# Kernel optimization log

Hardware: AMD Instinct MI355X
Metric: run time of the kernel (lower is better)

Reference implementation:

```python
import jax, jax.numpy as jnp
import numpy as np

N_NODES = 100000
N_EDGES = 1600000
IN_F = 128
OUT_F = 32
HEADS = 2
NEG_SLOPE = 0.2  # DGL GATConv default leaky_relu negative slope


def setup_inputs() -> dict:
    key = jax.random.key(0)
    ks = jax.random.split(key, 12)
    x = jax.random.normal(ks[0], (N_NODES, IN_F), dtype=jnp.float32)
    src = jax.random.randint(ks[1], (N_EDGES,), 0, N_NODES, dtype=jnp.int32)
    dst = jax.random.randint(ks[2], (N_EDGES,), 0, N_NODES, dtype=jnp.int32)
    # GATConv params: fc weight [IN_F, HEADS*OUT_F], attn_l/attn_r [HEADS, OUT_F], bias [HEADS*OUT_F]
    s = 1.0 / np.sqrt(IN_F)
    W = jax.random.normal(ks[3], (IN_F, HEADS * OUT_F), dtype=jnp.float32) * s
    attn_l = jax.random.normal(ks[4], (HEADS, OUT_F), dtype=jnp.float32) * s
    attn_r = jax.random.normal(ks[5], (HEADS, OUT_F), dtype=jnp.float32) * s
    bias_gat = jnp.zeros((HEADS * OUT_F,), dtype=jnp.float32)
    # MLPPredictor: lin1 (2*OUT_F -> OUT_F), lin2 (OUT_F -> 1)
    s1 = 1.0 / np.sqrt(2 * OUT_F)
    W1 = jax.random.normal(ks[6], (2 * OUT_F, OUT_F), dtype=jnp.float32) * s1
    b1 = jnp.zeros((OUT_F,), dtype=jnp.float32)
    s2 = 1.0 / np.sqrt(OUT_F)
    W2 = jax.random.normal(ks[7], (OUT_F, 1), dtype=jnp.float32) * s2
    b2 = jnp.zeros((1,), dtype=jnp.float32)
    return {"x": x, "W": W, "attn_l": attn_l, "attn_r": attn_r,
            "bias_gat": bias_gat, "W1": W1, "b1": b1, "W2": W2, "b2": b2,
            "src": src, "dst": dst}


def _forward(x, W, attn_l, attn_r, bias_gat, W1, b1, W2, b2, src, dst):
    # --- GATConv(in, out, 2 heads) ---
    feat = (x @ W).reshape(N_NODES, HEADS, OUT_F)           # [N,H,F]
    el = jnp.einsum('nhf,hf->nh', feat, attn_l)             # [N,H]
    er = jnp.einsum('nhf,hf->nh', feat, attn_r)             # [N,H]
    e = jax.nn.leaky_relu(el[src] + er[dst], NEG_SLOPE)     # [E,H]
    # edge softmax over incoming edges of each dst node (numerically stable)
    m = jax.ops.segment_max(e, dst, num_segments=N_NODES)   # [N,H]
    ex = jnp.exp(e - m[dst])                                # [E,H]
    denom = jax.ops.segment_sum(ex, dst, num_segments=N_NODES)  # [N,H]
    alpha = ex / denom[dst]                                 # [E,H]
    msg = feat[src] * alpha[:, :, None]                     # [E,H,F]
    rst = jax.ops.segment_sum(msg, dst, num_segments=N_NODES)   # [N,H,F]
    rst = rst + bias_gat.reshape(HEADS, OUT_F)
    h = jax.nn.relu(jnp.mean(rst, axis=1))                  # [N,F]
    # --- MLPPredictor: per-edge concat(src,dst) -> lin1 -> lin2 (no activation) ---
    hcat = jnp.concatenate([h[src], h[dst]], axis=1)        # [E,2F]
    score = (hcat @ W1 + b1) @ W2 + b2                      # [E,1]
    return score


def reference(x, W, attn_l, attn_r, bias_gat, W1, b1, W2, b2, src, dst):
    return _forward(x, W, attn_l, attn_r, bias_gat, W1, b1, W2, b2, src, dst)
```

## Files before the change

kernel.cpp:

```cpp
#include <hip/hip_runtime.h>
#include <hip/hip_fp16.h>

#define N_NODES 100000
#define N_EDGES 1600000
#define IN_F 128
#define OUT_F 32
#define HEADS 2
#define HO 64

#define NBUCK2 1563
#define BIN_BLOCKS 256
#define BIN_THREADS 1024
#define EPB (N_EDGES / BIN_BLOCKS)
#define NPT 7
#define LCAPH 1216

typedef __attribute__((ext_vector_type(8))) _Float16 half8;
typedef __attribute__((ext_vector_type(4))) _Float16 half4v;
typedef __attribute__((ext_vector_type(4))) float    f32x4;

#define XPAD 136

__global__ __launch_bounds__(256) void feat_k(
                       const float* __restrict__ x, const float* __restrict__ W,
                       const float* __restrict__ attn_l, const float* __restrict__ attn_r,
                       __half* __restrict__ feat16, float* __restrict__ el, float* __restrict__ er){
  __shared__ __align__(16) _Float16 Ws[64*XPAD];
  __shared__ __align__(16) _Float16 xs[64*XPAD];
  int tid = threadIdx.x;
  int node0 = blockIdx.x*64;

  for (int i = tid; i < 2048; i += 256){
    int k = i >> 4, c4 = (i & 15)*4;
    float4 v = ((const float4*)W)[i];
    Ws[(c4+0)*XPAD + k] = (_Float16)v.x;
    Ws[(c4+1)*XPAD + k] = (_Float16)v.y;
    Ws[(c4+2)*XPAD + k] = (_Float16)v.z;
    Ws[(c4+3)*XPAD + k] = (_Float16)v.w;
  }
  for (int i = tid; i < 2048; i += 256){
    int ln = i >> 5, kq = i & 31;
    int n = node0 + ln;
    float4 v = (n < N_NODES) ? ((const float4*)x)[(size_t)n*32 + kq]
                             : make_float4(0.f,0.f,0.f,0.f);
    half4v hv = { (_Float16)v.x, (_Float16)v.y, (_Float16)v.z, (_Float16)v.w };
    *(half4v*)&xs[ln*XPAD + kq*4] = hv;
  }
  __syncthreads();

  int w = tid >> 6, lane = tid & 63;
  int row_base = w*16;
  int lr = lane & 15, lg = lane >> 4;
  f32x4 acc0 = {0.f,0.f,0.f,0.f}, acc1 = {0.f,0.f,0.f,0.f};
  f32x4 acc2 = {0.f,0.f,0.f,0.f}, acc3 = {0.f,0.f,0.f,0.f};

  #pragma unroll
  for (int kk = 0; kk < 4; ++kk){
    int ko = kk*32 + lg*8;
    half8 a  = *(const half8*)&xs[(row_base + lr)*XPAD + ko];
    half8 b0 = *(const half8*)&Ws[( 0 + lr)*XPAD + ko];
    half8 b1 = *(const half8*)&Ws[(16 + lr)*XPAD + ko];
    half8 b2 = *(const half8*)&Ws[(32 + lr)*XPAD + ko];
    half8 b3 = *(const half8*)&Ws[(48 + lr)*XPAD + ko];
    acc0 = __builtin_amdgcn_mfma_f32_16x16x32_f16(a, b0, acc0, 0, 0, 0);
    acc1 = __builtin_amdgcn_mfma_f32_16x16x32_f16(a, b1, acc1, 0, 0, 0);
    acc2 = __builtin_amdgcn_mfma_f32_16x16x32_f16(a, b2, acc2, 0, 0, 0);
    acc3 = __builtin_amdgcn_mfma_f32_16x16x32_f16(a, b3, acc3, 0, 0, 0);
  }

  float al0 = attn_l[ 0 + lr], al1 = attn_l[16 + lr];
  float al2 = attn_l[32 + lr], al3 = attn_l[48 + lr];
  float ar0 = attn_r[ 0 + lr], ar1 = attn_r[16 + lr];
  float ar2 = attn_r[32 + lr], ar3 = attn_r[48 + lr];

  #pragma unroll
  for (int r = 0; r < 4; ++r){
    int n = node0 + row_base + lg*4 + r;
    float f0 = acc0[r], f1 = acc1[r], f2 = acc2[r], f3 = acc3[r];
    float p0 = f0*al0 + f1*al1, p1 = f2*al2 + f3*al3;
    float q0 = f0*ar0 + f1*ar1, q1 = f2*ar2 + f3*ar3;
    #pragma unroll
    for (int off = 1; off < 16; off <<= 1){
      p0 += __shfl_xor(p0, off); p1 += __shfl_xor(p1, off);
      q0 += __shfl_xor(q0, off); q1 += __shfl_xor(q1, off);
    }
    if (n < N_NODES){
      size_t base = (size_t)n*HO;
      feat16[base +  0 + lr] = __float2half_rn(f0);
      feat16[base + 16 + lr] = __float2half_rn(f1);
      feat16[base + 32 + lr] = __float2half_rn(f2);
      feat16[base + 48 + lr] = __float2half_rn(f3);
      if (lr == 0){
        *(float2*)&el[n*HEADS] = make_float2(p0, p1);
        *(float2*)&er[n*HEADS] = make_float2(q0, q1);
      }
    }
  }
}

__global__ __launch_bounds__(1024) void binB_k(const int* __restrict__ src,
                      const int* __restrict__ dst,
                      const float* __restrict__ el, const float* __restrict__ er,
                      const float* __restrict__ b1, const float* __restrict__ W2,
                      const float* __restrict__ b2,
                      int* __restrict__ bstart, float* __restrict__ ccomb,
                      uint2* __restrict__ stg){
  __shared__ int cnt[NBUCK2];
  int tid = threadIdx.x, blk = blockIdx.x;
  int lane = tid & 63, w = tid >> 6;
  if (blk == 0 && tid == 0){
    float a = 0.f;
    for (int k = 0; k < OUT_F; ++k) a = fmaf(b1[k], W2[k], a);
    *ccomb = a + b2[0];
  }
  for (int i = tid; i < NBUCK2; i += BIN_THREADS) cnt[i] = 0;
  __syncthreads();

  unsigned rx[NPT], rex[NPT];
  int rb[NPT];
  int ebase = blk*EPB;
  #pragma unroll
  for (int u = 0; u < NPT; ++u){
    int idx = tid + u*BIN_THREADS;
    rb[u] = -1;
    if (idx < EPB){
      int s = src[ebase + idx];
      int d = dst[ebase + idx];
      float2 elv = *(const float2*)&el[s*HEADS];
      float2 erv = *(const float2*)&er[d*HEADS];
      float t0 = elv.x + erv.x, t1 = elv.y + erv.y;
      t0 = t0 > 0.f ? t0 : 0.2f*t0;
      t1 = t1 > 0.f ? t1 : 0.2f*t1;
      __half2 ex2 = __float22half2_rn(make_float2(__expf(t0), __expf(t1)));
      int b = d >> 6;
      rb[u] = b;
      rx[u] = ((unsigned)s << 6) | (unsigned)(d & 63);
      rex[u] = *(const unsigned*)&ex2;
      atomicAdd(&cnt[b], 1);
    }
  }
  __syncthreads();

  if (w == 0){
    int run = 0;
    for (int c = 0; c < NBUCK2; c += 64){
      int i = c + lane;
      int v = (i < NBUCK2) ? cnt[i] : 0;
      int inc = v;
      #pragma unroll
      for (int off = 1; off < 64; off <<= 1){
        int t = __shfl_up(inc, off);
        if (lane >= off) inc += t;
      }
      if (i < NBUCK2) cnt[i] = run + inc - v;
      run += __shfl(inc, 63);
    }
  }
  __syncthreads();

  for (int i = tid; i < NBUCK2; i += BIN_THREADS)
    bstart[(size_t)blk*NBUCK2 + i] = cnt[i];
  __syncthreads();

  #pragma unroll
  for (int u = 0; u < NPT; ++u){
    if (rb[u] >= 0){
      int pos = atomicAdd(&cnt[rb[u]], 1);
      stg[(size_t)blk*EPB + pos] = make_uint2(rx[u], rex[u]);
    }
  }
}

__global__ void __launch_bounds__(512, 8) scatter_agg_k(
                              const int* __restrict__ bstart, const uint2* __restrict__ stg,
                              const __half* __restrict__ feat16, const float* __restrict__ bias,
                              const float* __restrict__ W1, const float* __restrict__ W2,
                              float* __restrict__ s1, float* __restrict__ s2){
  __shared__ uint2 lsev[LCAPH];
  __shared__ int soff[BIN_BLOCKS];
  __shared__ int send[BIN_BLOCKS];
  __shared__ float wc[64];
  __shared__ int hist[64];
  __shared__ int start_[64];
  __shared__ int cur[64];
  int b = blockIdx.x;
  int tid = threadIdx.x;
  int w = tid >> 6, lane = tid & 63;
  if (tid < 64){
    hist[tid] = 0;
    float a = 0.f;
    #pragma unroll
    for (int k = 0; k < OUT_F; ++k) a = fmaf(W1[tid*OUT_F + k], W2[k], a);
    wc[tid] = a;
  }
  for (int i = tid; i < BIN_BLOCKS; i += 512){
    int o = bstart[(size_t)i*NBUCK2 + b];
    int e = (b == NBUCK2-1) ? EPB : bstart[(size_t)i*NBUCK2 + b + 1];
    soff[i] = o; send[i] = e;
  }
  __syncthreads();

  int grp = tid >> 3, gl = tid & 7;

  for (int sg = grp; sg < BIN_BLOCKS; sg += 64){
    const uint2* seg = stg + (size_t)sg*EPB;
    int e = send[sg];
    for (int j = soff[sg] + gl; j < e; j += 8)
      atomicAdd(&hist[seg[j].x & 63], 1);
  }
  __syncthreads();

  if (tid < 64){
    int v = hist[tid];
    int inc = v;
    #pragma unroll
    for (int off = 1; off < 64; off <<= 1){
      int t = __shfl_up(inc, off);
      if (lane >= off) inc += t;
    }
    start_[tid] = inc - v;
    cur[tid] = inc - v;
  }
  __syncthreads();

  for (int sg = grp; sg < BIN_BLOCKS; sg += 64){
    const uint2* seg = stg + (size_t)sg*EPB;
    int e = send[sg];
    for (int j = soff[sg] + gl; j < e; j += 8){
      uint2 r = seg[j];
      int pos = atomicAdd(&cur[r.x & 63], 1);
      if (pos < LCAPH) lsev[pos] = make_uint2(r.x >> 6, r.y);
    }
  }
  __syncthreads();

  int g  = lane >> 4;
  int c4 = lane & 15;
  int h  = (c4 >= 8);
  float b0v = bias[c4*4 + 0], b1v = bias[c4*4 + 1], b2v = bias[c4*4 + 2], b3v = bias[c4*4 + 3];
  int f0 = (c4 & 7)*4;
  int wo = (h ? 32 : 0) + f0;
  float m0 = wc[wo], m1 = wc[wo+1], m2 = wc[wo+2], m3 = wc[wo+3];
  for (int i = 0; i < 8; ++i){
    int nl = w*8 + i;
    int node = b*64 + nl;
    if (node >= N_NODES) break;
    int s0 = start_[nl];
    int e0 = cur[nl]; if (e0 > LCAPH) e0 = LCAPH;
    int deg = e0 - s0; if (deg < 0) deg = 0;

    float a0=0.f, a1=0.f, a2=0.f, a3=0.f, dn=0.f;
    for (int j0 = 0; j0 < deg; j0 += 16){
      int jA = j0 + g, jB = j0 + 4 + g, jC = j0 + 8 + g, jD = j0 + 12 + g;
      float alA=0.f, alB=0.f, alC=0.f, alD=0.f;
      int snA=0, snB=0, snC=0, snD=0;
      if (jA < deg){ uint2 r = lsev[s0+jA]; snA = r.x;
        float2 e = __half22float2(*(const __half2*)&r.y); alA = (h?e.y:e.x); }
      if (jB < deg){ uint2 r = lsev[s0+jB]; snB = r.x;
        float2 e = __half22float2(*(const __half2*)&r.y); alB = (h?e.y:e.x); }
      if (jC < deg){ uint2 r = lsev[s0+jC]; snC = r.x;
        float2 e = __half22float2(*(const __half2*)&r.y); alC = (h?e.y:e.x); }
      if (jD < deg){ uint2 r = lsev[s0+jD]; snD = r.x;
        float2 e = __half22float2(*(const __half2*)&r.y); alD = (h?e.y:e.x); }
      dn += alA + alB + alC + alD;
      uint2 vA = *(const uint2*)(feat16 + (size_t)snA*HO + c4*4);
      uint2 vB = *(const uint2*)(feat16 + (size_t)snB*HO + c4*4);
      uint2 vC = *(const uint2*)(feat16 + (size_t)snC*HO + c4*4);
      uint2 vD = *(const uint2*)(feat16 + (size_t)snD*HO + c4*4);
      float2 fA01 = __half22float2(*(const __half2*)&vA.x);
      float2 fA23 = __half22float2(*(const __half2*)&vA.y);
      float2 fB01 = __half22float2(*(const __half2*)&vB.x);
      float2 fB23 = __half22float2(*(const __half2*)&vB.y);
      float2 fC01 = __half22float2(*(const __half2*)&vC.x);
      float2 fC23 = __half22float2(*(const __half2*)&vC.y);
      float2 fD01 = __half22float2(*(const __half2*)&vD.x);
      float2 fD23 = __half22float2(*(const __half2*)&vD.y);
      a0 = fmaf(alA, fA01.x, a0); a0 = fmaf(alB, fB01.x, a0);
      a0 = fmaf(alC, fC01.x, a0); a0 = fmaf(alD, fD01.x, a0);
      a1 = fmaf(alA, fA01.y, a1); a1 = fmaf(alB, fB01.y, a1);
      a1 = fmaf(alC, fC01.y, a1); a1 = fmaf(alD, fD01.y, a1);
      a2 = fmaf(alA, fA23.x, a2); a2 = fmaf(alB, fB23.x, a2);
      a2 = fmaf(alC, fC23.x, a2); a2 = fmaf(alD, fD23.x, a2);
      a3 = fmaf(alA, fA23.y, a3); a3 = fmaf(alB, fB23.y, a3);
      a3 = fmaf(alC, fC23.y, a3); a3 = fmaf(alD, fD23.y, a3);
    }
    a0 += __shfl_xor(a0, 16); a1 += __shfl_xor(a1, 16);
    a2 += __shfl_xor(a2, 16); a3 += __shfl_xor(a3, 16);
    dn += __shfl_xor(dn, 16);
    a0 += __shfl_xor(a0, 32); a1 += __shfl_xor(a1, 32);
    a2 += __shfl_xor(a2, 32); a3 += __shfl_xor(a3, 32);
    dn += __shfl_xor(dn, 32);
    float rh = dn > 0.f ? 1.f/dn : 0.f;
    a0 = fmaf(a0, rh, b0v); a1 = fmaf(a1, rh, b1v);
    a2 = fmaf(a2, rh, b2v); a3 = fmaf(a3, rh, b3v);
    float h0 = 0.5f*(a0 + __shfl_xor(a0, 8)); h0 = fmaxf(h0, 0.f);
    float h1 = 0.5f*(a1 + __shfl_xor(a1, 8)); h1 = fmaxf(h1, 0.f);
    float h2 = 0.5f*(a2 + __shfl_xor(a2, 8)); h2 = fmaxf(h2, 0.f);
    float h3 = 0.5f*(a3 + __shfl_xor(a3, 8)); h3 = fmaxf(h3, 0.f);
    float r = h0*m0 + h1*m1 + h2*m2 + h3*m3;
    r += __shfl_xor(r, 4); r += __shfl_xor(r, 2); r += __shfl_xor(r, 1);
    if (lane == 0)      s1[node] = r;
    else if (lane == 8) s2[node] = r;
  }
}

__global__ void edge_score_k(const int* __restrict__ src, const int* __restrict__ dst,
                             const float* __restrict__ s1, const float* __restrict__ s2,
                             const float* __restrict__ ccomb, float* __restrict__ out){
  int i = blockIdx.x*blockDim.x + threadIdx.x;
  if (i >= N_EDGES/4) return;
  int4 s4 = ((const int4*)src)[i];
  int4 d4 = ((const int4*)dst)[i];
  float c = ccomb[0];
  float4 o;
  o.x = s1[s4.x] + s2[d4.x] + c;
  o.y = s1[s4.y] + s2[d4.y] + c;
  o.z = s1[s4.z] + s2[d4.z] + c;
  o.w = s1[s4.w] + s2[d4.w] + c;
  ((float4*)out)[i] = o;
}

extern "C" void kernel_launch(void* const* d_in, const int* in_sizes, int n_in,
                              void* d_out, int out_size, void* d_ws, size_t ws_size,
                              hipStream_t stream){
  const float* x      = (const float*)d_in[0];
  const float* W      = (const float*)d_in[1];
  const float* attn_l = (const float*)d_in[2];
  const float* attn_r = (const float*)d_in[3];
  const float* bias   = (const float*)d_in[4];
  const float* W1     = (const float*)d_in[5];
  const float* b1     = (const float*)d_in[6];
  const float* W2     = (const float*)d_in[7];
  const float* b2     = (const float*)d_in[8];
  const int*   src    = (const int*)d_in[9];
  const int*   dst    = (const int*)d_in[10];
  float* out = (float*)d_out;

  float* ws = (float*)d_ws;
  size_t off = 0;
  __half* feat16 = (__half*)(ws + off); off += (size_t)N_NODES*HO/2;
  float*  el     = ws + off; off += (size_t)N_NODES*HEADS;
  float*  er     = ws + off; off += (size_t)N_NODES*HEADS;
  float*  s1     = ws + off; off += N_NODES;
  float*  s2     = ws + off; off += N_NODES;
  float*  ccomb  = ws + off; off += 64;
  int*    bstart = (int*)(ws + off); off += (size_t)BIN_BLOCKS*NBUCK2;
  off = (off + 1) & ~(size_t)1;
  uint2*  stg    = (uint2*)(ws + off); off += (size_t)2*N_EDGES;

  feat_k<<<(N_NODES + 63)/64, 256, 0, stream>>>(x, W, attn_l, attn_r, feat16, el, er);
  binB_k<<<BIN_BLOCKS, BIN_THREADS, 0, stream>>>(src, dst, el, er, b1, W2, b2,
                                                 bstart, ccomb, stg);
  scatter_agg_k<<<NBUCK2, 512, 0, stream>>>(bstart, stg, feat16, bias, W1, W2, s1, s2);
  edge_score_k<<<(N_EDGES/4 + 255)/256, 256, 0, stream>>>(src, dst, s1, s2, ccomb, out);
}
```

Before: 223.3 us.

## Vectorize binning loads, stage bucket edges once in LDS, widen edge-score kernel

The binning kernel now uses 250 blocks so each block's edge count splits evenly into int4 loads of src/dst, and it batches all gather loads before computing. The scatter-aggregate kernel computes per-segment offsets with a prefix scan and copies staged edges into LDS once. It then builds the histogram and does the local counting sort from LDS, where before it read global memory twice. The edge-score kernel processes eight edges per thread, and address math uses 32-bit shifts. This adds LDS usage (a second LCAPH buffer), which may reduce occupancy of the aggregate kernel.

Measured after the change: 220.3 us. Within noise of the previous version (-1.3%).

```diff
diff --git a/kernel.cpp b/kernel.cpp
--- a/kernel.cpp
+++ b/kernel.cpp
@@ -9,10 +9,10 @@
 #define HO 64
 
 #define NBUCK2 1563
-#define BIN_BLOCKS 256
+#define BIN_BLOCKS 250
 #define BIN_THREADS 1024
 #define EPB (N_EDGES / BIN_BLOCKS)
-#define NPT 7
+#define NV4 (EPB/4)
 #define LCAPH 1216
 
 typedef __attribute__((ext_vector_type(8))) _Float16 half8;
@@ -116,27 +116,40 @@
   for (int i = tid; i < NBUCK2; i += BIN_THREADS) cnt[i] = 0;
   __syncthreads();
 
-  unsigned rx[NPT], rex[NPT];
-  int rb[NPT];
-  int ebase = blk*EPB;
-  #pragma unroll
-  for (int u = 0; u < NPT; ++u){
-    int idx = tid + u*BIN_THREADS;
-    rb[u] = -1;
-    if (idx < EPB){
-      int s = src[ebase + idx];
-      int d = dst[ebase + idx];
-      float2 elv = *(const float2*)&el[s*HEADS];
-      float2 erv = *(const float2*)&er[d*HEADS];
-      float t0 = elv.x + erv.x, t1 = elv.y + erv.y;
+  int s_[8], d_[8];
+  int ne = 0;
+  const int4* s4p = (const int4*)(src + blk*EPB);
+  const int4* d4p = (const int4*)(dst + blk*EPB);
+  #pragma unroll
+  for (int u = 0; u < 2; ++u){
+    int i4 = tid + u*BIN_THREADS;
+    if (i4 < NV4){
+      int4 sv = s4p[i4], dv = d4p[i4];
+      s_[4*u+0]=sv.x; s_[4*u+1]=sv.y; s_[4*u+2]=sv.z; s_[4*u+3]=sv.w;
+      d_[4*u+0]=dv.x; d_[4*u+1]=dv.y; d_[4*u+2]=dv.z; d_[4*u+3]=dv.w;
+      ne = 4*u+4;
+    }
+  }
+  float2 elv[8], erv[8];
+  #pragma unroll
+  for (int i = 0; i < 8; ++i){
+    if (i < ne){
+      elv[i] = *(const float2*)&el[s_[i]*HEADS];
+      erv[i] = *(const float2*)&er[d_[i]*HEADS];
+    }
+  }
+  unsigned rx[8], rex[8]; int rb[8];
+  #pragma unroll
+  for (int i = 0; i < 8; ++i){
+    if (i < ne){
+      float t0 = elv[i].x + erv[i].x, t1 = elv[i].y + erv[i].y;
       t0 = t0 > 0.f ? t0 : 0.2f*t0;
       t1 = t1 > 0.f ? t1 : 0.2f*t1;
       __half2 ex2 = __float22half2_rn(make_float2(__expf(t0), __expf(t1)));
-      int b = d >> 6;
-      rb[u] = b;
-      rx[u] = ((unsigned)s << 6) | (unsigned)(d & 63);
-      rex[u] = *(const unsigned*)&ex2;
-      atomicAdd(&cnt[b], 1);
+      rb[i] = d_[i] >> 6;
+      rx[i] = ((unsigned)s_[i] << 6) | (unsigned)(d_[i] & 63);
+      rex[i] = *(const unsigned*)&ex2;
+      atomicAdd(&cnt[rb[i]], 1);
     }
   }
   __syncthreads();
@@ -163,10 +176,10 @@
   __syncthreads();
 
   #pragma unroll
-  for (int u = 0; u < NPT; ++u){
-    if (rb[u] >= 0){
-      int pos = atomicAdd(&cnt[rb[u]], 1);
-      stg[(size_t)blk*EPB + pos] = make_uint2(rx[u], rex[u]);
+  for (int i = 0; i < 8; ++i){
+    if (i < ne){
+      int pos = atomicAdd(&cnt[rb[i]], 1);
+      stg[(size_t)blk*EPB + pos] = make_uint2(rx[i], rex[i]);
     }
   }
 }
@@ -176,13 +189,16 @@
                               const __half* __restrict__ feat16, const float* __restrict__ bias,
                               const float* __restrict__ W1, const float* __restrict__ W2,
                               float* __restrict__ s1, float* __restrict__ s2){
+  __shared__ uint2 lraw[LCAPH];
   __shared__ uint2 lsev[LCAPH];
   __shared__ int soff[BIN_BLOCKS];
   __shared__ int send[BIN_BLOCKS];
+  __shared__ int segb[BIN_BLOCKS];
   __shared__ float wc[64];
   __shared__ int hist[64];
   __shared__ int start_[64];
   __shared__ int cur[64];
+  __shared__ int wtot[4];
   int b = blockIdx.x;
   int tid = threadIdx.x;
   int w = tid >> 6, lane = tid & 63;
@@ -200,37 +216,62 @@
   }
   __syncthreads();
 
-  int grp = tid >> 3, gl = tid & 7;
-
-  for (int sg = grp; sg < BIN_BLOCKS; sg += 64){
-    const uint2* seg = stg + (size_t)sg*EPB;
-    int e = send[sg];
-    for (int j = soff[sg] + gl; j < e; j += 8)
-      atomicAdd(&hist[seg[j].x & 63], 1);
-  }
-  __syncthreads();
-
-  if (tid < 64){
-    int v = hist[tid];
-    int inc = v;
+  int c_ = 0, inc = 0;
+  if (tid < 256){
+    if (tid < BIN_BLOCKS) c_ = send[tid] - soff[tid];
+    inc = c_;
     #pragma unroll
     for (int off = 1; off < 64; off <<= 1){
       int t = __shfl_up(inc, off);
       if (lane >= off) inc += t;
     }
-    start_[tid] = inc - v;
-    cur[tid] = inc - v;
-  }
-  __syncthreads();
-
+    if (lane == 63) wtot[w] = inc;
+  }
+  __syncthreads();
+  if (tid == 0){
+    int r = 0;
+    #pragma unroll
+    for (int i2 = 0; i2 < 4; ++i2){ int t = wtot[i2]; wtot[i2] = r; r += t; }
+  }
+  __syncthreads();
+  if (tid < BIN_BLOCKS) segb[tid] = wtot[w] + inc - c_;
+  __syncthreads();
+
+  int grp = tid >> 3, gl = tid & 7;
   for (int sg = grp; sg < BIN_BLOCKS; sg += 64){
     const uint2* seg = stg + (size_t)sg*EPB;
-    int e = send[sg];
-    for (int j = soff[sg] + gl; j < e; j += 8){
+    int o = soff[sg], e = send[sg];
+    int base = segb[sg] - o;
+    for (int j = o + gl; j < e; j += 8){
       uint2 r = seg[j];
-      int pos = atomicAdd(&cur[r.x & 63], 1);
-      if (pos < LCAPH) lsev[pos] = make_uint2(r.x >> 6, r.y);
-    }
+      int p = base + j;
+      if (p < LCAPH){
+        lraw[p] = r;
+        atomicAdd(&hist[r.x & 63], 1);
+      }
+    }
+  }
+  __syncthreads();
+
+  if (tid < 64){
+    int v = hist[tid];
+    int inc2 = v;
+    #pragma unroll
+    for (int off = 1; off < 64; off <<= 1){
+      int t = __shfl_up(inc2, off);
+      if (lane >= off) inc2 += t;
+    }
+    start_[tid] = inc2 - v;
+    cur[tid] = inc2 - v;
+  }
+  __syncthreads();
+
+  int tot = segb[BIN_BLOCKS-1] + (send[BIN_BLOCKS-1] - soff[BIN_BLOCKS-1]);
+  if (tot > LCAPH) tot = LCAPH;
+  for (int i = tid; i < tot; i += 512){
+    uint2 r = lraw[i];
+    int pos = atomicAdd(&cur[r.x & 63], 1);
+    lsev[pos] = make_uint2(r.x >> 6, r.y);
   }
   __syncthreads();
 
@@ -241,6 +282,7 @@
   int f0 = (c4 & 7)*4;
   int wo = (h ? 32 : 0) + f0;
   float m0 = wc[wo], m1 = wc[wo+1], m2 = wc[wo+2], m3 = wc[wo+3];
+  unsigned co = (unsigned)(c4*4);
   for (int i = 0; i < 8; ++i){
     int nl = w*8 + i;
     int node = b*64 + nl;
@@ -253,20 +295,20 @@
     for (int j0 = 0; j0 < deg; j0 += 16){
       int jA = j0 + g, jB = j0 + 4 + g, jC = j0 + 8 + g, jD = j0 + 12 + g;
       float alA=0.f, alB=0.f, alC=0.f, alD=0.f;
-      int snA=0, snB=0, snC=0, snD=0;
+      unsigned snA=0, snB=0, snC=0, snD=0;
       if (jA < deg){ uint2 r = lsev[s0+jA]; snA = r.x;
-        float2 e = __half22float2(*(const __half2*)&r.y); alA = (h?e.y:e.x); }
+        alA = __half2float(((const __half*)&r.y)[h]); }
       if (jB < deg){ uint2 r = lsev[s0+jB]; snB = r.x;
-        float2 e = __half22float2(*(const __half2*)&r.y); alB = (h?e.y:e.x); }
+        alB = __half2float(((const __half*)&r.y)[h]); }
       if (jC < deg){ uint2 r = lsev[s0+jC]; snC = r.x;
-        float2 e = __half22float2(*(const __half2*)&r.y); alC = (h?e.y:e.x); }
+        alC = __half2float(((const __half*)&r.y)[h]); }
       if (jD < deg){ uint2 r = lsev[s0+jD]; snD = r.x;
-        float2 e = __half22float2(*(const __half2*)&r.y); alD = (h?e.y:e.x); }
+        alD = __half2float(((const __half*)&r.y)[h]); }
       dn += alA + alB + alC + alD;
-      uint2 vA = *(const uint2*)(feat16 + (size_t)snA*HO + c4*4);
-      uint2 vB = *(const uint2*)(feat16 + (size_t)snB*HO + c4*4);
-      uint2 vC = *(const uint2*)(feat16 + (size_t)snC*HO + c4*4);
-      uint2 vD = *(const uint2*)(feat16 + (size_t)snD*HO + c4*4);
+      uint2 vA = *(const uint2*)(feat16 + ((snA << 6) + co));
+      uint2 vB = *(const uint2*)(feat16 + ((snB << 6) + co));
+      uint2 vC = *(const uint2*)(feat16 + ((snC << 6) + co));
+      uint2 vD = *(const uint2*)(feat16 + ((snD << 6) + co));
       float2 fA01 = __half22float2(*(const __half2*)&vA.x);
       float2 fA23 = __half22float2(*(const __half2*)&vA.y);
       float2 fB01 = __half22float2(*(const __half2*)&vB.x);
@@ -304,20 +346,24 @@
   }
 }
 
-__global__ void edge_score_k(const int* __restrict__ src, const int* __restrict__ dst,
+__global__ __launch_bounds__(256) void edge_score_k(
+                             const int* __restrict__ src, const int* __restrict__ dst,
                              const float* __restrict__ s1, const float* __restrict__ s2,
                              const float* __restrict__ ccomb, float* __restrict__ out){
   int i = blockIdx.x*blockDim.x + threadIdx.x;
-  if (i >= N_EDGES/4) return;
-  int4 s4 = ((const int4*)src)[i];
-  int4 d4 = ((const int4*)dst)[i];
+  if (i >= N_EDGES/8) return;
+  int4 sa = ((const int4*)src)[2*i],   sb = ((const int4*)src)[2*i+1];
+  int4 da = ((const int4*)dst)[2*i],   db = ((const int4*)dst)[2*i+1];
+  float v0 = s1[sa.x], v1 = s1[sa.y], v2 = s1[sa.z], v3 = s1[sa.w];
+  float v4 = s1[sb.x], v5 = s1[sb.y], v6 = s1[sb.z], v7 = s1[sb.w];
+  float u0 = s2[da.x], u1 = s2[da.y], u2 = s2[da.z], u3 = s2[da.w];
+  float u4 = s2[db.x], u5 = s2[db.y], u6 = s2[db.z], u7 = s2[db.w];
   float c = ccomb[0];
-  float4 o;
-  o.x = s1[s4.x] + s2[d4.x] + c;
-  o.y = s1[s4.y] + s2[d4.y] + c;
-  o.z = s1[s4.z] + s2[d4.z] + c;
-  o.w = s1[s4.w] + s2[d4.w] + c;
-  ((float4*)out)[i] = o;
+  float4 oa, ob;
+  oa.x = v0+u0+c; oa.y = v1+u1+c; oa.z = v2+u2+c; oa.w = v3+u3+c;
+  ob.x = v4+u4+c; ob.y = v5+u5+c; ob.z = v6+u6+c; ob.w = v7+u7+c;
+  ((float4*)out)[2*i]   = oa;
+  ((float4*)out)[2*i+1] = ob;
 }
 
 extern "C" void kernel_launch(void* const* d_in, const int* in_sizes, int n_in,
@@ -352,5 +398,5 @@
   binB_k<<<BIN_BLOCKS, BIN_THREADS, 0, stream>>>(src, dst, el, er, b1, W2, b2,
                                                  bstart, ccomb, stg);
   scatter_agg_k<<<NBUCK2, 512, 0, stream>>>(bstart, stg, feat16, bias, W1, W2, s1, s2);
-  edge_score_k<<<(N_EDGES/4 + 255)/256, 256, 0, stream>>>(src, dst, s1, s2, ccomb, out);
+  edge_score_k<<<(N_EDGES/8 + 255)/256, 256, 0, stream>>>(src, dst, s1, s2, ccomb, out);
 }
```
